# Kernel optimization log

Measured on AMD Instinct MI355X. Metric: run time of the kernel, lower is better.

The kernel has to match this reference:

```python
import jax, jax.numpy as jnp
import numpy as np

INPUT_SIZE = 768
HIDDEN = 384


def _gru_dir(x, W_ih, W_hh, b_ih, b_hh, reverse):
    """Single-direction GRU, torch gate order (r, z, n).
    x: [B, S, D] -> outputs [B, S, H]."""
    B = x.shape[0]
    H = W_hh.shape[1]
    # Precompute input projections for all timesteps: [B, S, 3H] -> [S, B, 3H]
    xw = jnp.swapaxes(x @ W_ih.T + b_ih, 0, 1)

    def step(h, xw_t):
        gh = h @ W_hh.T + b_hh
        xr, xz, xn = jnp.split(xw_t, 3, axis=-1)
        hr, hz, hn = jnp.split(gh, 3, axis=-1)
        r = jax.nn.sigmoid(xr + hr)
        z = jax.nn.sigmoid(xz + hz)
        n = jnp.tanh(xn + r * hn)
        h_new = (1.0 - z) * n + z * h
        return h_new, h_new

    h0 = jnp.zeros((B, H), dtype=x.dtype)
    _, hs = jax.lax.scan(step, h0, xw, reverse=reverse)  # [S, B, H]
    return jnp.swapaxes(hs, 0, 1)


def setup_inputs() -> dict:
    key = jax.random.key(0)
    ks = jax.random.split(key, 12)
    B, S, D, H = 32, 512, INPUT_SIZE, HIDDEN
    s_ih = 1.0 / np.sqrt(H)
    u = lambda k, shape: jax.random.uniform(k, shape, jnp.float32, -s_ih, s_ih)
    inp = {
        "ip": jax.random.normal(ks[0], (B, S, D), jnp.float32),
        # forward-direction GRU params
        "W_ih_f": u(ks[1], (3 * H, D)),
        "W_hh_f": u(ks[2], (3 * H, H)),
        "b_ih_f": u(ks[3], (3 * H,)),
        "b_hh_f": u(ks[4], (3 * H,)),
        # backward-direction GRU params
        "W_ih_b": u(ks[5], (3 * H, D)),
        "W_hh_b": u(ks[6], (3 * H, H)),
        "b_ih_b": u(ks[7], (3 * H,)),
        "b_hh_b": u(ks[8], (3 * H,)),
        # sentence attention params (input_dim = 2H)
        "W_attn": u(ks[9], (2 * H, 2 * H)),
        "b_attn": u(ks[10], (2 * H,)),
        "context": jax.random.normal(ks[11], (2 * H,), jnp.float32) * 0.05,
    }
    return inp


def reference(ip, W_ih_f, W_hh_f, b_ih_f, b_hh_f,
              W_ih_b, W_hh_b, b_ih_b, b_hh_b,
              W_attn, b_attn, context):
    # BiGRU encode: concat forward & backward hidden states -> [B, S, 2H]
    h_f = _gru_dir(ip, W_ih_f, W_hh_f, b_ih_f, b_hh_f, reverse=False)
    h_b = _gru_dir(ip, W_ih_b, W_hh_b, b_ih_b, b_hh_b, reverse=True)
    out = jnp.concatenate([h_f, h_b], axis=-1)
    # Additive attention pooling over sentences
    scores = jnp.tanh(out @ W_attn.T + b_attn) @ context  # [B, S]
    attn = jax.nn.softmax(scores, axis=1)
    doc_embeds = jnp.einsum("bs,bsd->bd", attn, out)  # [B, 2H]
    return doc_embeds
```

## Files before the change

kernel.cpp:

```cpp
#include <hip/hip_runtime.h>
#include <hip/hip_fp16.h>

typedef _Float16 half2_t __attribute__((ext_vector_type(2)));
typedef _Float16 half4_t __attribute__((ext_vector_type(4)));
typedef _Float16 half8_t __attribute__((ext_vector_type(8)));
typedef float floatx4 __attribute__((ext_vector_type(4)));

#define B_   32
#define S_   512
#define D_   768
#define H_   384
#define H3_  1152
#define M_   (B_*S_)
#define N2_  (2*H3_)
#define TWOH_ 768
#define NWG_DIR 6
#define JSPAN 64

__device__ __forceinline__ int4 load16_cc(const void* p) {
  int4 r;
  unsigned long long a = (unsigned long long)p;
  asm volatile("global_load_dwordx4 %0, %1, off sc0 sc1\n\t"
               "s_waitcnt vmcnt(0)"
               : "=v"(r) : "v"(a) : "memory");
  return r;
}
__device__ __forceinline__ void load16_cc3(const void* p0, const void* p1, const void* p2,
                                           int4& v0, int4& v1, int4& v2) {
  unsigned long long a0 = (unsigned long long)p0;
  unsigned long long a1 = (unsigned long long)p1;
  unsigned long long a2 = (unsigned long long)p2;
  asm volatile("global_load_dwordx4 %0, %3, off sc0 sc1\n\t"
               "global_load_dwordx4 %1, %4, off sc0 sc1\n\t"
               "global_load_dwordx4 %2, %5, off sc0 sc1\n\t"
               "s_waitcnt vmcnt(0)"
               : "=&v"(v0), "=&v"(v1), "=&v"(v2)
               : "v"(a0), "v"(a1), "v"(a2) : "memory");
}
__device__ __forceinline__ void store8_cc(void* p, int2 v) {
  unsigned long long a = (unsigned long long)p;
  asm volatile("global_store_dwordx2 %0, %1, off sc0 sc1" :: "v"(a), "v"(v) : "memory");
}
__device__ __forceinline__ void store4_cc(void* p, int d) {
  unsigned long long a = (unsigned long long)p;
  asm volatile("global_store_dword %0, %1, off sc0 sc1" :: "v"(a), "v"(d) : "memory");
}
__device__ __forceinline__ void wait_vm0() {
  asm volatile("s_waitcnt vmcnt(0)" ::: "memory");
}

__global__ void cvt_f32_f16_kernel(const float* __restrict__ src,
                                   _Float16* __restrict__ dst, int n4) {
  int i = blockIdx.x * blockDim.x + threadIdx.x;
  if (i >= n4) return;
  float4 v = ((const float4*)src)[i];
  half4_t h = {(_Float16)v.x, (_Float16)v.y, (_Float16)v.z, (_Float16)v.w};
  ((half4_t*)dst)[i] = h;
}

__global__ __launch_bounds__(256) void gemm_xw_kernel(
    const _Float16* __restrict__ A, const _Float16* __restrict__ Bm,
    const float* __restrict__ bias_f, const float* __restrict__ bias_b,
    _Float16* __restrict__ xw) {
  __shared__ _Float16 As[64][40];
  __shared__ _Float16 Bs[64][40];
  const int m0 = blockIdx.x * 64, n0 = blockIdx.y * 64;
  const int tid = threadIdx.x, lane = tid & 63, w = tid >> 6;
  const int wm = w >> 1, wn = w & 1;
  const int q = lane >> 4, c = lane & 15;
  floatx4 acc[2][2] = {};

  const int t = tid & 127;
  const int srow = t >> 1, skh = (t & 1) * 16;
  const _Float16* gsrc =
      (tid < 128 ? A + (size_t)(m0 + srow) * D_ : Bm + (size_t)(n0 + srow) * D_) + skh;
  _Float16* ldst = (tid < 128) ? &As[srow][skh] : &Bs[srow][skh];

  for (int k0 = 0; k0 < D_; k0 += 32) {
    half8_t v0 = *(const half8_t*)(gsrc + k0);
    half8_t v1 = *(const half8_t*)(gsrc + k0 + 8);
    __syncthreads();
    *(half8_t*)ldst = v0;
    *(half8_t*)(ldst + 8) = v1;
    __syncthreads();
    half8_t a0 = *(const half8_t*)&As[wm * 32 + c][q * 8];
    half8_t a1 = *(const half8_t*)&As[wm * 32 + 16 + c][q * 8];
    half8_t b0 = *(const half8_t*)&Bs[wn * 32 + c][q * 8];
    half8_t b1 = *(const half8_t*)&Bs[wn * 32 + 16 + c][q * 8];
    acc[0][0] = __builtin_amdgcn_mfma_f32_16x16x32_f16(a0, b0, acc[0][0], 0, 0, 0);
    acc[0][1] = __builtin_amdgcn_mfma_f32_16x16x32_f16(a0, b1, acc[0][1], 0, 0, 0);
    acc[1][0] = __builtin_amdgcn_mfma_f32_16x16x32_f16(a1, b0, acc[1][0], 0, 0, 0);
    acc[1][1] = __builtin_amdgcn_mfma_f32_16x16x32_f16(a1, b1, acc[1][1], 0, 0, 0);
  }
  for (int mi = 0; mi < 2; ++mi)
    for (int ni = 0; ni < 2; ++ni)
      for (int r = 0; r < 4; ++r) {
        int m = m0 + wm * 32 + mi * 16 + q * 4 + r;
        int n = n0 + wn * 32 + ni * 16 + c;
        int dir = n >= H3_;
        int nn = n - dir * H3_;
        float bv = dir ? bias_b[nn] : bias_f[nn];
        float vv = acc[mi][ni][r] + bv;
        int s = m & (S_ - 1), bb = m >> 9;
        xw[(((size_t)dir * S_ + s) * B_ + bb) * H3_ + nn] = (_Float16)vv;
      }
}

__global__ __launch_bounds__(512, 1) void gru_mfma_kernel(
    const _Float16* __restrict__ xw,
    const _Float16* __restrict__ Whh,
    const float* __restrict__ bhh_f, const float* __restrict__ bhh_b,
    _Float16* __restrict__ hglob,
    _Float16* __restrict__ out16,
    int* __restrict__ bar) {
  const int wg = blockIdx.x;
  const int dir = wg / NWG_DIR;
  const int wgj = wg % NWG_DIR;
  const int j0w = wgj * JSPAN;
  const int tid = threadIdx.x, lane = tid & 63, w = tid >> 6;
  const int bt = w & 1, jt = w >> 1;
  const int c = lane & 15, q = lane >> 4;

  __shared__ __align__(16) _Float16 hS[32 * 392];

  half8_t bfr[3][12];
  {
    const int jglob = j0w + jt * 16 + c;
#pragma unroll
    for (int g = 0; g < 3; ++g) {
      const _Float16* wp = Whh + ((size_t)dir * H3_ + g * H_ + jglob) * H_ + q * 8;
#pragma unroll
      for (int kt = 0; kt < 12; ++kt) bfr[g][kt] = *(const half8_t*)(wp + kt * 32);
    }
  }
  const float* bhh = dir ? bhh_b : bhh_f;
  const int bl = bt * 16 + c;
  const int jg4 = j0w + jt * 16 + q * 4;
  const float4 br4 = *(const float4*)&bhh[jg4];
  const float4 bz4 = *(const float4*)&bhh[H_ + jg4];
  const float4 bn4 = *(const float4*)&bhh[2 * H_ + jg4];
  float hc[4] = {0.f, 0.f, 0.f, 0.f};

  int* const flg = bar + dir * 64;
  const int fw = wgj * 8 + w;
  const int* fpoll = flg + ((lane < 12) ? lane * 4 : 0);

  for (int step = 0; step < S_; ++step) {
    const int t = dir ? (S_ - 1 - step) : step;
    const int par = step & 1;

    const _Float16* xbase = xw + (((size_t)dir * S_ + t) * B_ + bl) * H3_ + jg4;
    half4_t xr4 = *(const half4_t*)(xbase);
    half4_t xz4 = *(const half4_t*)(xbase + H_);
    half4_t xn4 = *(const half4_t*)(xbase + 2 * H_);

    if (step == 0) {
      for (int i = tid; i < 32 * 392 / 2; i += 512) ((int*)hS)[i] = 0;
    } else {
      for (;;) {
        int4 f = load16_cc(fpoll);
        bool ok = (lane >= 12) ||
                  (f.x >= step && f.y >= step && f.z >= step && f.w >= step);
        if (__all(ok)) break;
      }
      const _Float16* hb = hglob + ((size_t)dir * 2 + par) * B_ * H_;
      int g0 = tid, g1 = tid + 512, g2 = tid + 1024;
      int4 v0, v1, v2;
      load16_cc3(hb + (g0 / 48) * H_ + (g0 % 48) * 8,
                 hb + (g1 / 48) * H_ + (g1 % 48) * 8,
                 hb + (g2 / 48) * H_ + (g2 % 48) * 8, v0, v1, v2);
      *(int4*)&hS[(g0 / 48) * 392 + (g0 % 48) * 8] = v0;
      *(int4*)&hS[(g1 / 48) * 392 + (g1 % 48) * 8] = v1;
      *(int4*)&hS[(g2 / 48) * 392 + (g2 % 48) * 8] = v2;
    }
    __syncthreads();

    floatx4 a0 = {}, a1 = {}, a2 = {};
    {
      const _Float16* hrow = &hS[(bt * 16 + c) * 392 + q * 8];
#pragma unroll
      for (int kt = 0; kt < 12; ++kt) {
        half8_t hf = *(const half8_t*)(hrow + kt * 32);
        a0 = __builtin_amdgcn_mfma_f32_16x16x32_f16(bfr[0][kt], hf, a0, 0, 0, 0);
        a1 = __builtin_amdgcn_mfma_f32_16x16x32_f16(bfr[1][kt], hf, a1, 0, 0, 0);
        a2 = __builtin_amdgcn_mfma_f32_16x16x32_f16(bfr[2][kt], hf, a2, 0, 0, 0);
      }
    }

    half4_t hh;
#pragma unroll
    for (int r = 0; r < 4; ++r) {
      float rr = 1.f / (1.f + __expf(-((float)xr4[r] + a0[r] + br4[r])));
      float zz = 1.f / (1.f + __expf(-((float)xz4[r] + a1[r] + bz4[r])));
      float u = (float)xn4[r] + rr * (a2[r] + bn4[r]);
      float e = __expf(-2.f * u);
      float nv = (1.f - e) / (1.f + e);
      hc[r] = (1.f - zz) * nv + zz * hc[r];
      hh[r] = (_Float16)hc[r];
    }
    _Float16* hdst = hglob + (((size_t)dir * 2 + (par ^ 1)) * B_ + bl) * H_ + jg4;
    store8_cc(hdst, __builtin_bit_cast(int2, hh));
    wait_vm0();
    if (lane == 0) store4_cc(flg + fw, step + 1);
    *(half4_t*)&out16[((size_t)bl * S_ + t) * TWOH_ + dir * H_ + jg4] = hh;
  }
}

__global__ __launch_bounds__(256) void attn_score_kernel(
    const _Float16* __restrict__ A ,
    const _Float16* __restrict__ Bm ,
    const float* __restrict__ b_attn, const float* __restrict__ ctx,
    float* __restrict__ scores) {
  __shared__ _Float16 As[64][40];
  __shared__ _Float16 Bs[64][40];
  const int m0 = blockIdx.x * 64, n0 = blockIdx.y * 64;
  const int tid = threadIdx.x, lane = tid & 63, w = tid >> 6;
  const int wm = w >> 1, wn = w & 1;
  const int q = lane >> 4, c = lane & 15;
  floatx4 acc[2][2] = {};

  const int t = tid & 127;
  const int srow = t >> 1, skh = (t & 1) * 16;
  const _Float16* gsrc =
      (tid < 128 ? A + (size_t)(m0 + srow) * D_ : Bm + (size_t)(n0 + srow) * D_) + skh;
  _Float16* ldst = (tid < 128) ? &As[srow][skh] : &Bs[srow][skh];

  for (int k0 = 0; k0 < D_; k0 += 32) {
    half8_t v0 = *(const half8_t*)(gsrc + k0);
    half8_t v1 = *(const half8_t*)(gsrc + k0 + 8);
    __syncthreads();
    *(half8_t*)ldst = v0;
    *(half8_t*)(ldst + 8) = v1;
    __syncthreads();
    half8_t a0 = *(const half8_t*)&As[wm * 32 + c][q * 8];
    half8_t a1 = *(const half8_t*)&As[wm * 32 + 16 + c][q * 8];
    half8_t b0 = *(const half8_t*)&Bs[wn * 32 + c][q * 8];
    half8_t b1 = *(const half8_t*)&Bs[wn * 32 + 16 + c][q * 8];
    acc[0][0] = __builtin_amdgcn_mfma_f32_16x16x32_f16(a0, b0, acc[0][0], 0, 0, 0);
    acc[0][1] = __builtin_amdgcn_mfma_f32_16x16x32_f16(a0, b1, acc[0][1], 0, 0, 0);
    acc[1][0] = __builtin_amdgcn_mfma_f32_16x16x32_f16(a1, b0, acc[1][0], 0, 0, 0);
    acc[1][1] = __builtin_amdgcn_mfma_f32_16x16x32_f16(a1, b1, acc[1][1], 0, 0, 0);
  }
  for (int mi = 0; mi < 2; ++mi)
    for (int ni = 0; ni < 2; ++ni)
      for (int r = 0; r < 4; ++r) {
        int n = n0 + wn * 32 + ni * 16 + c;
        float vv = tanhf(acc[mi][ni][r] + b_attn[n]) * ctx[n];
        vv += __shfl_xor(vv, 1);
        vv += __shfl_xor(vv, 2);
        vv += __shfl_xor(vv, 4);
        vv += __shfl_xor(vv, 8);
        if (c == 0) {
          int m = m0 + wm * 32 + mi * 16 + q * 4 + r;
          atomicAdd(&scores[m], vv);
        }
      }
}

__global__ __launch_bounds__(256) void softmax_kernel(const float* __restrict__ scores,
                                                      float* __restrict__ attn) {
  const int b = blockIdx.x, tid = threadIdx.x;
  __shared__ float red[8];
  float s0 = scores[b * S_ + tid], s1 = scores[b * S_ + 256 + tid];
  float m = fmaxf(s0, s1);
  for (int off = 1; off < 64; off <<= 1) m = fmaxf(m, __shfl_xor(m, off));
  int wv = tid >> 6;
  if ((tid & 63) == 0) red[wv] = m;
  __syncthreads();
  m = fmaxf(fmaxf(red[0], red[1]), fmaxf(red[2], red[3]));
  float e0 = expf(s0 - m), e1 = expf(s1 - m);
  float sum = e0 + e1;
  for (int off = 1; off < 64; off <<= 1) sum += __shfl_xor(sum, off);
  if ((tid & 63) == 0) red[4 + wv] = sum;
  __syncthreads();
  sum = red[4] + red[5] + red[6] + red[7];
  float inv = 1.0f / sum;
  attn[b * S_ + tid] = e0 * inv;
  attn[b * S_ + 256 + tid] = e1 * inv;
}

__global__ __launch_bounds__(384) void doc_kernel(const float* __restrict__ attn,
                                                  const _Float16* __restrict__ out16,
                                                  float* __restrict__ dout) {
  const int b = blockIdx.x, tid = threadIdx.x;
  __shared__ float at[S_];
  for (int i = tid; i < S_; i += 384) at[i] = attn[b * S_ + i];
  __syncthreads();
  const half2_t* p = (const half2_t*)(out16 + (size_t)b * S_ * TWOH_) + tid;
  float acc0 = 0.f, acc1 = 0.f;
  for (int s = 0; s < S_; ++s) {
    half2_t h = p[(size_t)s * (TWOH_ / 2)];
    float wgt = at[s];
    acc0 += wgt * (float)h.x;
    acc1 += wgt * (float)h.y;
  }
  dout[b * TWOH_ + tid * 2] = acc0;
  dout[b * TWOH_ + tid * 2 + 1] = acc1;
}

extern "C" void kernel_launch(void* const* d_in, const int* in_sizes, int n_in,
                              void* d_out, int out_size, void* d_ws, size_t ws_size,
                              hipStream_t stream) {
  const float* ip     = (const float*)d_in[0];
  const float* W_ih_f = (const float*)d_in[1];
  const float* W_hh_f = (const float*)d_in[2];
  const float* b_ih_f = (const float*)d_in[3];
  const float* b_hh_f_p = (const float*)d_in[4];
  const float* W_ih_b = (const float*)d_in[5];
  const float* W_hh_b = (const float*)d_in[6];
  const float* b_ih_b = (const float*)d_in[7];
  const float* b_hh_b_p = (const float*)d_in[8];
  const float* W_attn = (const float*)d_in[9];
  const float* b_attn = (const float*)d_in[10];
  const float* context = (const float*)d_in[11];
  float* doc = (float*)d_out;

  char* ws = (char*)d_ws;
  size_t off = 0;
  auto alloc = [&](size_t bytes) {
    char* p = ws + off;
    off += (bytes + 255) & ~(size_t)255;
    return p;
  };
  _Float16* ip16    = (_Float16*)alloc((size_t)M_ * D_ * 2);
  _Float16* Wih16   = (_Float16*)alloc((size_t)N2_ * D_ * 2);
  _Float16* Whh16   = (_Float16*)alloc((size_t)2 * H3_ * H_ * 2);
  _Float16* Wattn16 = (_Float16*)alloc((size_t)TWOH_ * TWOH_ * 2);
  _Float16* xw      = (_Float16*)alloc((size_t)2 * S_ * B_ * H3_ * 2);
  _Float16* out16   = (_Float16*)alloc((size_t)B_ * S_ * TWOH_ * 2);
  _Float16* hglob   = (_Float16*)alloc((size_t)2 * 2 * B_ * H_ * 2);
  int*      bar     = (int*)alloc(4096);
  float* scores     = (float*)alloc((size_t)M_ * 4);
  float* attn       = (float*)alloc((size_t)M_ * 4);

  cvt_f32_f16_kernel<<<(M_ * D_ / 4 + 255) / 256, 256, 0, stream>>>(ip, ip16, M_ * D_ / 4);
  cvt_f32_f16_kernel<<<(H3_ * D_ / 4 + 255) / 256, 256, 0, stream>>>(W_ih_f, Wih16, H3_ * D_ / 4);
  cvt_f32_f16_kernel<<<(H3_ * D_ / 4 + 255) / 256, 256, 0, stream>>>(W_ih_b, Wih16 + (size_t)H3_ * D_, H3_ * D_ / 4);
  cvt_f32_f16_kernel<<<(H3_ * H_ / 4 + 255) / 256, 256, 0, stream>>>(W_hh_f, Whh16, H3_ * H_ / 4);
  cvt_f32_f16_kernel<<<(H3_ * H_ / 4 + 255) / 256, 256, 0, stream>>>(W_hh_b, Whh16 + (size_t)H3_ * H_, H3_ * H_ / 4);
  cvt_f32_f16_kernel<<<(TWOH_ * TWOH_ / 4 + 255) / 256, 256, 0, stream>>>(W_attn, Wattn16, TWOH_ * TWOH_ / 4);

  gemm_xw_kernel<<<dim3(M_ / 64, N2_ / 64), 256, 0, stream>>>(ip16, Wih16, b_ih_f, b_ih_b, xw);

  hipMemsetAsync(hglob, 0, (size_t)2 * 2 * B_ * H_ * 2, stream);
  hipMemsetAsync(bar, 0, 4096, stream);
  {
    const _Float16* xw_a = xw;
    const _Float16* whh_a = Whh16;
    const float* bf_a = b_hh_f_p;
    const float* bb_a = b_hh_b_p;
    _Float16* hg_a = hglob;
    _Float16* o16_a = out16;
    int* bar_a = bar;
    void* args[] = {(void*)&xw_a, (void*)&whh_a, (void*)&bf_a, (void*)&bb_a,
                    (void*)&hg_a, (void*)&o16_a, (void*)&bar_a};
    hipLaunchCooperativeKernel((const void*)gru_mfma_kernel, dim3(2 * NWG_DIR),
                               dim3(512), args, 0, stream);
  }

  hipMemsetAsync(scores, 0, (size_t)M_ * 4, stream);
  attn_score_kernel<<<dim3(M_ / 64, TWOH_ / 64), 256, 0, stream>>>(out16, Wattn16, b_attn, context, scores);

  softmax_kernel<<<B_, 256, 0, stream>>>(scores, attn);
  doc_kernel<<<B_, 384, 0, stream>>>(attn, out16, doc);
}
```

Measured before the change: 2.526 ms.

## Use per-workgroup atomic flags and lighter cache scope in GRU step sync

```diff
diff --git a/kernel.cpp b/kernel.cpp
--- a/kernel.cpp
+++ b/kernel.cpp
@@ -17,33 +17,21 @@
 #define NWG_DIR 6
 #define JSPAN 64
 
-__device__ __forceinline__ int4 load16_cc(const void* p) {
-  int4 r;
-  unsigned long long a = (unsigned long long)p;
-  asm volatile("global_load_dwordx4 %0, %1, off sc0 sc1\n\t"
-               "s_waitcnt vmcnt(0)"
-               : "=v"(r) : "v"(a) : "memory");
-  return r;
-}
 __device__ __forceinline__ void load16_cc3(const void* p0, const void* p1, const void* p2,
                                            int4& v0, int4& v1, int4& v2) {
   unsigned long long a0 = (unsigned long long)p0;
   unsigned long long a1 = (unsigned long long)p1;
   unsigned long long a2 = (unsigned long long)p2;
-  asm volatile("global_load_dwordx4 %0, %3, off sc0 sc1\n\t"
-               "global_load_dwordx4 %1, %4, off sc0 sc1\n\t"
-               "global_load_dwordx4 %2, %5, off sc0 sc1\n\t"
+  asm volatile("global_load_dwordx4 %0, %3, off sc1\n\t"
+               "global_load_dwordx4 %1, %4, off sc1\n\t"
+               "global_load_dwordx4 %2, %5, off sc1\n\t"
                "s_waitcnt vmcnt(0)"
                : "=&v"(v0), "=&v"(v1), "=&v"(v2)
                : "v"(a0), "v"(a1), "v"(a2) : "memory");
 }
 __device__ __forceinline__ void store8_cc(void* p, int2 v) {
   unsigned long long a = (unsigned long long)p;
-  asm volatile("global_store_dwordx2 %0, %1, off sc0 sc1" :: "v"(a), "v"(v) : "memory");
-}
-__device__ __forceinline__ void store4_cc(void* p, int d) {
-  unsigned long long a = (unsigned long long)p;
-  asm volatile("global_store_dword %0, %1, off sc0 sc1" :: "v"(a), "v"(d) : "memory");
+  asm volatile("global_store_dwordx2 %0, %1, off sc1" :: "v"(a), "v"(v) : "memory");
 }
 __device__ __forceinline__ void wait_vm0() {
   asm volatile("s_waitcnt vmcnt(0)" ::: "memory");
@@ -106,7 +94,7 @@
       }
 }
 
-__global__ __launch_bounds__(512, 1) void gru_mfma_kernel(
+__global__ __launch_bounds__(512, 2) void gru_mfma_kernel(
     const _Float16* __restrict__ xw,
     const _Float16* __restrict__ Whh,
     const float* __restrict__ bhh_f, const float* __restrict__ bhh_b,
@@ -141,9 +129,7 @@
   const float4 bn4 = *(const float4*)&bhh[2 * H_ + jg4];
   float hc[4] = {0.f, 0.f, 0.f, 0.f};
 
-  int* const flg = bar + dir * 64;
-  const int fw = wgj * 8 + w;
-  const int* fpoll = flg + ((lane < 12) ? lane * 4 : 0);
+  int* flg = bar + dir * 256;
 
   for (int step = 0; step < S_; ++step) {
     const int t = dir ? (S_ - 1 - step) : step;
@@ -154,15 +140,18 @@
     half4_t xz4 = *(const half4_t*)(xbase + H_);
     half4_t xn4 = *(const half4_t*)(xbase + 2 * H_);
 
-    if (step == 0) {
-      for (int i = tid; i < 32 * 392 / 2; i += 512) ((int*)hS)[i] = 0;
-    } else {
-      for (;;) {
-        int4 f = load16_cc(fpoll);
-        bool ok = (lane >= 12) ||
-                  (f.x >= step && f.y >= step && f.z >= step && f.w >= step);
-        if (__all(ok)) break;
-      }
+    if (step > 0 && w == 0) {
+      int v;
+      do {
+        v = (lane < NWG_DIR)
+                ? __hip_atomic_load(&flg[lane * 16], __ATOMIC_RELAXED,
+                                    __HIP_MEMORY_SCOPE_AGENT)
+                : 0x7fffffff;
+      } while (!__all(v >= step));
+    }
+    __syncthreads();
+
+    {
       const _Float16* hb = hglob + ((size_t)dir * 2 + par) * B_ * H_;
       int g0 = tid, g1 = tid + 512, g2 = tid + 1024;
       int4 v0, v1, v2;
@@ -198,10 +187,13 @@
       hc[r] = (1.f - zz) * nv + zz * hc[r];
       hh[r] = (_Float16)hc[r];
     }
-    _Float16* hdst = hglob + (((size_t)dir * 2 + (par ^ 1)) * B_ + bl) * H_ + jg4;
-    store8_cc(hdst, __builtin_bit_cast(int2, hh));
+    store8_cc(hglob + (((size_t)dir * 2 + (par ^ 1)) * B_ + bl) * H_ + jg4,
+              __builtin_bit_cast(int2, hh));
     wait_vm0();
-    if (lane == 0) store4_cc(flg + fw, step + 1);
+    __syncthreads();
+    if (tid == 0)
+      __hip_atomic_store(&flg[wgj * 16], step + 1, __ATOMIC_RELAXED,
+                         __HIP_MEMORY_SCOPE_AGENT);
     *(half4_t*)&out16[((size_t)bl * S_ + t) * TWOH_ + dir * H_ + jg4] = hh;
   }
 }
```

After: 2.217 ms. 1.14x faster.
